# Kernel tuning notes

Measured on AMD Instinct MI355X. Metric: run time of the kernel, lower is better.

The kernel has to match this reference:

```python
import jax, jax.numpy as jnp
import numpy as np

NUM_HEADS = 24
HEAD_DIM = 64
SCALE = HEAD_DIM ** -0.5


def setup_inputs() -> dict:
    key = jax.random.key(0)
    ks = jax.random.split(key, 6)
    b, n_img, n_txt = 2, 4096, 128
    c_in, c_out, c_ctx = 1536, 1536, 4096
    x = jax.random.normal(ks[0], (b, n_img, c_in), dtype=jnp.float32)
    context = jax.random.normal(ks[1], (b, n_txt, c_ctx), dtype=jnp.float32)
    # realistic padding mask: first 96 of 128 tokens valid
    context_mask = jnp.broadcast_to(jnp.arange(n_txt) < 96, (b, n_txt))
    # Linear(in, out, bias=False) stored as [in, out] so y = x @ W
    Wq = jax.random.normal(ks[2], (c_in, c_out), dtype=jnp.float32) * (c_in ** -0.5)
    Wk = jax.random.normal(ks[3], (c_ctx, c_out), dtype=jnp.float32) * (c_ctx ** -0.5)
    Wv = jax.random.normal(ks[4], (c_ctx, c_out), dtype=jnp.float32) * (c_ctx ** -0.5)
    Wo = jax.random.normal(ks[5], (c_out, c_out), dtype=jnp.float32) * (c_out ** -0.5)
    return {"x": x, "context": context, "context_mask": context_mask,
            "Wq": Wq, "Wk": Wk, "Wv": Wv, "Wo": Wo}


def reference(x, context, context_mask, Wq, Wk, Wv, Wo):
    b, n, _ = x.shape
    h, d = NUM_HEADS, HEAD_DIM
    # project and split heads: b n (h d) -> b h n d
    q = (x @ Wq).reshape(b, n, h, d).transpose(0, 2, 1, 3)
    k = (context @ Wk).reshape(b, -1, h, d).transpose(0, 2, 1, 3)
    v = (context @ Wv).reshape(b, -1, h, d).transpose(0, 2, 1, 3)
    scores = jnp.einsum('bhid,bhjd->bhij', q, k) * SCALE
    max_neg = -jnp.finfo(scores.dtype).max
    scores = jnp.where(context_mask[:, None, None, :], scores, max_neg)
    attn = jax.nn.softmax(scores, axis=-1)
    out = jnp.einsum('bhij,bhjd->bhid', attn, v)
    out = out.transpose(0, 2, 1, 3).reshape(b, n, h * d)
    return out @ Wo
```

## Files before the change

### kernel.cpp

```cpp
#include <hip/hip_runtime.h>

typedef __attribute__((ext_vector_type(8))) short s8bf;
typedef __attribute__((ext_vector_type(8))) __bf16 v8bf;
typedef __attribute__((ext_vector_type(4))) float f32x4;

__device__ __forceinline__ short f2bf(float f) {
  union { float f; unsigned u; } v; v.f = f;
  unsigned r = v.u + 0x7FFFu + ((v.u >> 16) & 1u);
  return (short)(r >> 16);
}

__device__ __forceinline__ f32x4 mfma16(s8bf a, s8bf b, f32x4 c) {
  return __builtin_amdgcn_mfma_f32_16x16x32_bf16(
      __builtin_bit_cast(v8bf, a), __builtin_bit_cast(v8bf, b), c, 0, 0, 0);
}

__device__ __forceinline__ void gl_lds16(const void* g, void* l) {
  __builtin_amdgcn_global_load_lds(
      (const __attribute__((address_space(1))) unsigned*)g,
      (__attribute__((address_space(3))) unsigned*)l, 16, 0, 0);
}

__global__ void cvt_f32_bf16_k(const float* __restrict__ in, short* __restrict__ out, int n4) {
  int i = blockIdx.x * 256 + threadIdx.x;
  if (i < n4) {
    float4 v = ((const float4*)in)[i];
    short4 o;
    o.x = f2bf(v.x); o.y = f2bf(v.y); o.z = f2bf(v.z); o.w = f2bf(v.w);
    ((short4*)out)[i] = o;
  }
}

__global__ void transp_bf16_k(const float* __restrict__ W, short* __restrict__ Wt, int K, int N) {
  __shared__ float t[32][33];
  int k0 = blockIdx.x * 32, n0 = blockIdx.y * 32;
  int tx = threadIdx.x & 31, ty = threadIdx.x >> 5;
  #pragma unroll
  for (int i = 0; i < 4; ++i)
    t[ty + i * 8][tx] = W[(size_t)(k0 + ty + i * 8) * N + n0 + tx];
  __syncthreads();
  #pragma unroll
  for (int i = 0; i < 4; ++i)
    Wt[(size_t)(n0 + ty + i * 8) * K + k0 + tx] = f2bf(t[tx][ty + i * 8]);
}

__global__ void mask_bias_k(const void* __restrict__ mask, float* __restrict__ bias, int n) {
  __shared__ int fmt;
  const unsigned char* p8 = (const unsigned char*)mask;
  if (threadIdx.x == 0) {
    const float* pf = (const float*)mask;
    int allf = 1, anyone = 0;
    for (int i = 0; i < 64; ++i) {
      float f = pf[i];
      if (f != 0.0f && f != 1.0f) allf = 0;
      if (f == 1.0f) anyone = 1;
    }
    int any13 = 0;
    for (int i = 0; i < 256; ++i) if ((i & 3) && p8[i]) any13 = 1;
    fmt = (allf && anyone) ? 2 : (any13 ? 0 : 1);
  }
  __syncthreads();
  int j = threadIdx.x;
  if (j < n) {
    int m;
    if (fmt == 2)      m = (((const float*)mask)[j] != 0.0f);
    else if (fmt == 0) m = (p8[j] != 0);
    else               m = (((const int*)mask)[j] != 0);
    bias[j] = m ? 0.0f : -1e30f;
  }
}

template<int MODE>
__global__ __launch_bounds__(512, 2) void gemm8ph_k(
    const short* __restrict__ A, const short* __restrict__ Bt, void* __restrict__ C,
    int M, int N, int K)
{
  extern __shared__ char ldsb[];
  const int tid = threadIdx.x, wid = tid >> 6, lane = tid & 63;
  const int nbx = N / 192;
  const int nwg = gridDim.x, bid = blockIdx.x;
  const int swz = (bid & 7) * (nwg >> 3) + (bid >> 3);
  const int m0 = (swz / nbx) * 256, n0 = (swz % nbx) * 192;
  const int wm = wid >> 2, wn = wid & 3;
  const int NT = K / 64;

  const int sx  = (lane & 7) << 4;
  const int c0b = ((lane >> 4) * 16) ^ sx;
  const int c1b = ((lane >> 4) * 16 + 64) ^ sx;
  const int aoff0 = (wm * 128 + (lane & 15)) * 128 + c0b;
  const int aoff1 = (wm * 128 + (lane & 15)) * 128 + c1b;
  const int boff0 = 32768 + (wn * 48 + (lane & 15)) * 128 + c0b;
  const int boff1 = 32768 + (wn * 48 + (lane & 15)) * 128 + c1b;

  const int strow = tid >> 3;
  const int stcol = (16 * ((tid & 7) ^ ((tid >> 3) & 7))) >> 1;
  const short* sp[7];
  #pragma unroll
  for (int r = 0; r < 7; ++r) {
    if (r < 4) sp[r] = A  + (size_t)(m0 + r * 64 + strow) * K + stcol;
    else       sp[r] = Bt + (size_t)(n0 + (r - 4) * 64 + strow) * K + stcol;
  }

  f32x4 acc[8][3] = {};
  s8bf bfr[3][2];

  #pragma unroll
  for (int r = 0; r < 7; ++r) gl_lds16(sp[r], ldsb + r * 8192 + tid * 16);
  #pragma unroll
  for (int r = 0; r < 7; ++r) gl_lds16(sp[r] + 64, ldsb + 57344 + r * 8192 + tid * 16);
  asm volatile("s_waitcnt vmcnt(7)" ::: "memory");
  __builtin_amdgcn_s_barrier();

  for (int t = 0; t < NT; ++t) {
    const int bo = (t & 1) * 57344;
    const int so2 = ((t + 2) < NT ? (t + 2) : (NT - 1)) * 64;
    s8bf a0[4], a1[4], a2[4], a3[4];
    #pragma unroll
    for (int i = 0; i < 4; ++i) a0[i] = *(const s8bf*)(ldsb + bo + aoff0 + i * 2048);
    #pragma unroll
    for (int nf = 0; nf < 3; ++nf) bfr[nf][0] = *(const s8bf*)(ldsb + bo + boff0 + nf * 2048);
    #pragma unroll
    for (int i = 0; i < 4; ++i) a1[i] = *(const s8bf*)(ldsb + bo + aoff1 + i * 2048);
    #pragma unroll
    for (int nf = 0; nf < 3; ++nf) bfr[nf][1] = *(const s8bf*)(ldsb + bo + boff1 + nf * 2048);
    __builtin_amdgcn_s_barrier();
    asm volatile("s_waitcnt lgkmcnt(7)" ::: "memory");
    __builtin_amdgcn_s_setprio(1);
    #pragma unroll
    for (int i = 0; i < 4; ++i)
      #pragma unroll
      for (int nf = 0; nf < 3; ++nf)
        acc[i][nf] = mfma16(a0[i], bfr[nf][0], acc[i][nf]);
    __builtin_amdgcn_s_setprio(0);
    __builtin_amdgcn_s_barrier();
    #pragma unroll
    for (int i = 0; i < 4; ++i) a2[i] = *(const s8bf*)(ldsb + bo + aoff0 + (4 + i) * 2048);
    #pragma unroll
    for (int i = 0; i < 4; ++i) a3[i] = *(const s8bf*)(ldsb + bo + aoff1 + (4 + i) * 2048);
    __builtin_amdgcn_s_barrier();
    asm volatile("s_waitcnt lgkmcnt(8)" ::: "memory");
    __builtin_amdgcn_s_setprio(1);
    #pragma unroll
    for (int i = 0; i < 4; ++i)
      #pragma unroll
      for (int nf = 0; nf < 3; ++nf)
        acc[i][nf] = mfma16(a1[i], bfr[nf][1], acc[i][nf]);
    __builtin_amdgcn_s_setprio(0);
    asm volatile("s_waitcnt lgkmcnt(0)" ::: "memory");
    __builtin_amdgcn_s_barrier();
    #pragma unroll
    for (int r = 0; r < 4; ++r) gl_lds16(sp[r] + so2, ldsb + bo + r * 8192 + tid * 16);
    __builtin_amdgcn_s_barrier();
    __builtin_amdgcn_s_setprio(1);
    #pragma unroll
    for (int i = 0; i < 4; ++i)
      #pragma unroll
      for (int nf = 0; nf < 3; ++nf)
        acc[4 + i][nf] = mfma16(a2[i], bfr[nf][0], acc[4 + i][nf]);
    __builtin_amdgcn_s_setprio(0);
    __builtin_amdgcn_s_barrier();
    #pragma unroll
    for (int r = 4; r < 7; ++r) gl_lds16(sp[r] + so2, ldsb + bo + r * 8192 + tid * 16);
    __builtin_amdgcn_s_barrier();
    __builtin_amdgcn_s_setprio(1);
    #pragma unroll
    for (int i = 0; i < 4; ++i)
      #pragma unroll
      for (int nf = 0; nf < 3; ++nf)
        acc[4 + i][nf] = mfma16(a3[i], bfr[nf][1], acc[4 + i][nf]);
    __builtin_amdgcn_s_setprio(0);
    asm volatile("s_waitcnt vmcnt(7)" ::: "memory");
    __builtin_amdgcn_s_barrier();
  }
  asm volatile("s_waitcnt vmcnt(0)" ::: "memory");

  const int r0 = m0 + wm * 128 + ((lane >> 4) << 2);
  const int c0 = n0 + wn * 48 + (lane & 15);
  #pragma unroll
  for (int mf = 0; mf < 8; ++mf)
    #pragma unroll
    for (int nf = 0; nf < 3; ++nf)
      #pragma unroll
      for (int v = 0; v < 4; ++v) {
        int row = r0 + mf * 16 + v, col = c0 + nf * 16;
        float val = acc[mf][nf][v];
        if (MODE == 0) ((short*)C)[(size_t)row * N + col] = f2bf(val);
        else           ((float*)C)[(size_t)row * N + col] = val;
      }
}

template<int MODE>
__global__ __launch_bounds__(256, 2) void gemm_bt_k(
    const short* __restrict__ A, const short* __restrict__ Bt, void* __restrict__ C,
    int M, int N, int K, int kchunk)
{
  __shared__ short aT[128 * 32];
  __shared__ short bT[128 * 32];
  const int m0 = blockIdx.x * 128, n0 = blockIdx.y * 128;
  const int wid = threadIdx.x >> 6, lane = threadIdx.x & 63;
  const int wr = wid >> 1, wc = wid & 1;
  const int k_lo = blockIdx.z * kchunk, k_hi = k_lo + kchunk;
  f32x4 acc[4][4] = {};
  const int srow = wid * 32 + (lane >> 2);
  const int skoff = (lane & 3) * 8;
  const short* aG = A + (size_t)(m0 + srow) * K + skoff;
  const short* bG = Bt + (size_t)(n0 + srow) * K + skoff;
  char* aL = (char*)aT + wid * 2048;
  char* bL = (char*)bT + wid * 2048;
  const short* ap = aT + (wr * 64 + (lane & 15)) * 32 + (lane >> 4) * 8;
  const short* bp = bT + (wc * 64 + (lane & 15)) * 32 + (lane >> 4) * 8;
  for (int k0 = k_lo; k0 < k_hi; k0 += 32) {
    gl_lds16(aG + k0, aL);
    gl_lds16(aG + (size_t)16 * K + k0, aL + 1024);
    gl_lds16(bG + k0, bL);
    gl_lds16(bG + (size_t)16 * K + k0, bL + 1024);
    __syncthreads();
    s8bf af[4], bf[4];
    #pragma unroll
    for (int i = 0; i < 4; ++i) {
      af[i] = *(const s8bf*)(ap + i * 512);
      bf[i] = *(const s8bf*)(bp + i * 512);
    }
    #pragma unroll
    for (int mi = 0; mi < 4; ++mi)
      #pragma unroll
      for (int ni = 0; ni < 4; ++ni)
        acc[mi][ni] = mfma16(af[mi], bf[ni], acc[mi][ni]);
    __syncthreads();
  }
  const int r0 = m0 + wr * 64 + ((lane >> 4) << 2);
  const int c0 = n0 + wc * 64 + (lane & 15);
  float* Cf = (float*)C + (size_t)blockIdx.z * 786432;
  #pragma unroll
  for (int mi = 0; mi < 4; ++mi)
    #pragma unroll
    for (int ni = 0; ni < 4; ++ni)
      #pragma unroll
      for (int v = 0; v < 4; ++v) {
        int row = r0 + mi * 16 + v, col = c0 + ni * 16;
        Cf[(size_t)row * N + col] = acc[mi][ni][v];
      }
}

__global__ void kv_reduce_k(const float* __restrict__ part, short* __restrict__ kbf,
                            short* __restrict__ vtbf) {
  int t = blockIdx.x * 256 + threadIdx.x;
  int row = t / 768, c4 = (t % 768) * 4;
  float4 s = {0.f, 0.f, 0.f, 0.f};
  const float* p = part + (size_t)row * 3072 + c4;
  #pragma unroll
  for (int z = 0; z < 4; ++z) {
    float4 v = *(const float4*)(p + (size_t)z * 786432);
    s.x += v.x; s.y += v.y; s.z += v.z; s.w += v.w;
  }
  if (c4 < 1536) {
    short4 o = { f2bf(s.x), f2bf(s.y), f2bf(s.z), f2bf(s.w) };
    *(short4*)(kbf + (size_t)row * 1536 + c4) = o;
  } else {
    int b = row >> 7, j = row & 127, c = c4 - 1536;
    vtbf[((size_t)(b * 1536 + c + 0)) * 128 + j] = f2bf(s.x);
    vtbf[((size_t)(b * 1536 + c + 1)) * 128 + j] = f2bf(s.y);
    vtbf[((size_t)(b * 1536 + c + 2)) * 128 + j] = f2bf(s.z);
    vtbf[((size_t)(b * 1536 + c + 3)) * 128 + j] = f2bf(s.w);
  }
}

__global__ __launch_bounds__(256, 3) void attn_k(
    const short* __restrict__ q, const short* __restrict__ kk,
    const short* __restrict__ vt, const float* __restrict__ bias,
    short* __restrict__ ao)
{
  __shared__ char sm_[49152];
  const int it = blockIdx.x, h = blockIdx.y, b = blockIdx.z;
  const int wid = threadIdx.x >> 6, lane = threadIdx.x & 63;
  const int i0 = it * 128;
  char* kT = sm_;
  char* vT = sm_ + 16384;
  char* pB = (wid < 2) ? (sm_ + wid * 8192) : (sm_ + 16384 + wid * 8192);

  #pragma unroll
  for (int c = 0; c < 4; ++c) {
    int seg = c * 256 + wid * 64 + lane;
    int j = seg >> 3, ds = seg & 7;
    int dsrc = ds ^ (j & 7);
    gl_lds16(kk + ((size_t)(b * 128 + j) * 1536 + h * 64 + dsrc * 8),
             kT + c * 4096 + wid * 1024);
  }
  #pragma unroll
  for (int c = 0; c < 4; ++c) {
    int seg = c * 256 + wid * 64 + lane;
    int d = seg >> 4, js = seg & 15;
    int jsrc = js ^ (d & 7);
    gl_lds16(vt + ((size_t)(b * 1536 + h * 64 + d) * 128 + jsrc * 8),
             vT + c * 4096 + wid * 1024);
  }

  float bcol[8];
  #pragma unroll
  for (int nj = 0; nj < 8; ++nj) bcol[nj] = bias[b * 128 + nj * 16 + (lane & 15)];

  s8bf qf[2][2];
  #pragma unroll
  for (int mi = 0; mi < 2; ++mi)
    #pragma unroll
    for (int ks = 0; ks < 2; ++ks) {
      size_t row = (size_t)(b * 4096 + i0 + wid * 32 + mi * 16 + (lane & 15));
      qf[mi][ks] = *(const s8bf*)(q + row * 1536 + h * 64 + ks * 32 + (lane >> 4) * 8);
    }
  __syncthreads();

  f32x4 s[2][8] = {};
  #pragma unroll
  for (int ks = 0; ks < 2; ++ks) {
    int kd = ks * 32 + (lane >> 4) * 8;
    #pragma unroll
    for (int nj = 0; nj < 8; ++nj) {
      int j = nj * 16 + (lane & 15);
      s8bf kb = *(const s8bf*)(kT + j * 128 + ((2 * kd) ^ ((j & 7) << 4)));
      s[0][nj] = mfma16(qf[0][ks], kb, s[0][nj]);
      s[1][nj] = mfma16(qf[1][ks], kb, s[1][nj]);
    }
  }
  __syncthreads();

  float sm[2][4];
  #pragma unroll
  for (int mi = 0; mi < 2; ++mi)
    #pragma unroll
    for (int v = 0; v < 4; ++v) {
      float mx = -1e30f;
      #pragma unroll
      for (int nj = 0; nj < 8; ++nj) {
        float sv = s[mi][nj][v] * 0.125f + bcol[nj];
        s[mi][nj][v] = sv;
        mx = fmaxf(mx, sv);
      }
      mx = fmaxf(mx, __shfl_xor(mx, 1));
      mx = fmaxf(mx, __shfl_xor(mx, 2));
      mx = fmaxf(mx, __shfl_xor(mx, 4));
      mx = fmaxf(mx, __shfl_xor(mx, 8));
      float ss = 0.f;
      #pragma unroll
      for (int nj = 0; nj < 8; ++nj) {
        float p = __expf(s[mi][nj][v] - mx);
        s[mi][nj][v] = p;
        ss += p;
      }
      ss += __shfl_xor(ss, 1);
      ss += __shfl_xor(ss, 2);
      ss += __shfl_xor(ss, 4);
      ss += __shfl_xor(ss, 8);
      sm[mi][v] = ss;
    }

  #pragma unroll
  for (int mi = 0; mi < 2; ++mi)
    #pragma unroll
    for (int v = 0; v < 4; ++v) {
      int r = mi * 16 + ((lane >> 4) << 2) + v;
      char* base = pB + r * 256;
      #pragma unroll
      for (int nj = 0; nj < 8; ++nj) {
        int j = nj * 16 + (lane & 15);
        *(short*)(base + ((2 * j) ^ ((r & 7) << 4))) = f2bf(s[mi][nj][v]);
      }
    }
  __syncthreads();

  f32x4 o_[2][4] = {};
  #pragma unroll
  for (int ks = 0; ks < 4; ++ks) {
    int j = ks * 32 + (lane >> 4) * 8;
    s8bf pa[2];
    #pragma unroll
    for (int mi = 0; mi < 2; ++mi) {
      int r = mi * 16 + (lane & 15);
      pa[mi] = *(const s8bf*)(pB + r * 256 + ((2 * j) ^ ((r & 7) << 4)));
    }
    #pragma unroll
    for (int dj = 0; dj < 4; ++dj) {
      int d = dj * 16 + (lane & 15);
      s8bf vb = *(const s8bf*)(vT + d * 256 + ((2 * j) ^ ((d & 7) << 4)));
      o_[0][dj] = mfma16(pa[0], vb, o_[0][dj]);
      o_[1][dj] = mfma16(pa[1], vb, o_[1][dj]);
    }
  }

  #pragma unroll
  for (int mi = 0; mi < 2; ++mi)
    #pragma unroll
    for (int v = 0; v < 4; ++v) {
      int r = mi * 16 + ((lane >> 4) << 2) + v;
      float is = 1.0f / sm[mi][v];
      size_t row = (size_t)(b * 4096 + i0 + wid * 32 + r);
      #pragma unroll
      for (int dj = 0; dj < 4; ++dj) {
        int d = dj * 16 + (lane & 15);
        ao[row * 1536 + h * 64 + d] = f2bf(o_[mi][dj][v] * is);
      }
    }
}

extern "C" void kernel_launch(void* const* d_in, const int* in_sizes, int n_in,
                              void* d_out, int out_size, void* d_ws, size_t ws_size,
                              hipStream_t stream) {
  const float* x   = (const float*)d_in[0];
  const float* ctx = (const float*)d_in[1];
  const void*  msk = d_in[2];
  const float* Wq  = (const float*)d_in[3];
  const float* Wk  = (const float*)d_in[4];
  const float* Wv  = (const float*)d_in[5];
  const float* Wo  = (const float*)d_in[6];
  float* out = (float*)d_out;

  const int B = 2, NI = 4096, NT = 128, C = 1536, CC = 4096, H = 24;
  const int Mq = B * NI;
  const int Mk = B * NT;

  size_t off = 0;
  auto carve = [&](size_t bytes) -> void* {
    void* p = (char*)d_ws + off;
    off += (bytes + 255) & ~(size_t)255;
    return p;
  };
  short* xbf   = (short*)carve((size_t)Mq * C * 2);
  short* ctxbf = (short*)carve((size_t)Mk * CC * 2);
  short* WqT   = (short*)carve((size_t)C * C * 2);
  short* WkT   = (short*)carve((size_t)CC * C * 2);
  short* WvT   = (short*)carve((size_t)CC * C * 2);
  short* WoT   = (short*)carve((size_t)C * C * 2);
  short* qbf   = (short*)carve((size_t)Mq * C * 2);
  short* kbf   = (short*)carve((size_t)Mk * C * 2);
  short* vtbf  = (short*)carve((size_t)Mk * C * 2);
  float* bias  = (float*)carve(256 * 4);
  short* aout  = xbf;
  float* part  = out;

  hipFuncSetAttribute((const void*)gemm8ph_k<0>, hipFuncAttributeMaxDynamicSharedMemorySize, 114688);
  hipFuncSetAttribute((const void*)gemm8ph_k<1>, hipFuncAttributeMaxDynamicSharedMemorySize, 114688);

  cvt_f32_bf16_k<<<(Mq * C / 4 + 255) / 256, 256, 0, stream>>>(x, xbf, Mq * C / 4);
  cvt_f32_bf16_k<<<(Mk * CC / 4 + 255) / 256, 256, 0, stream>>>(ctx, ctxbf, Mk * CC / 4);
  transp_bf16_k<<<dim3(C / 32, C / 32), 256, 0, stream>>>(Wq, WqT, C, C);
  transp_bf16_k<<<dim3(CC / 32, C / 32), 256, 0, stream>>>(Wk, WkT, CC, C);
  transp_bf16_k<<<dim3(CC / 32, C / 32), 256, 0, stream>>>(Wv, WvT, CC, C);
  transp_bf16_k<<<dim3(C / 32, C / 32), 256, 0, stream>>>(Wo, WoT, C, C);
  mask_bias_k<<<1, 256, 0, stream>>>(msk, bias, 256);

  gemm8ph_k<0><<<(Mq / 256) * (C / 192), 512, 114688, stream>>>(xbf, WqT, qbf, Mq, C, C);
  gemm_bt_k<5><<<dim3(Mk / 128, 3072 / 128, 4), 256, 0, stream>>>(ctxbf, WkT, part, Mk, 3072, CC, 1024);
  kv_reduce_k<<<768, 256, 0, stream>>>(part, kbf, vtbf);

  attn_k<<<dim3(NI / 128, H, B), 256, 0, stream>>>(qbf, kbf, vtbf, bias, aout);

  gemm8ph_k<1><<<(Mq / 256) * (C / 192), 512, 114688, stream>>>(aout, WoT, out, Mq, C, C);
}
```

Baseline: 187.2 us.

## Rewrite projection GEMM with 256x256 tiles and four-phase split-K-half pipeline

Replaces the 256x192-tile eight-phase GEMM used for the Q and output projections with a 256x256-tile variant. This kernel splits each 64-wide K step into two 32-wide halves, each with its own XOR-swizzled LDS layout, and interleaves global-to-LDS prefetches of the next tiles between the MFMA phases. The larger N tile raises arithmetic intensity per LDS byte and reduces the workgroup count from 256 to 192. In exchange it uses 128 KB of LDS (possibly limiting occupancy to one block per CU), keeps more accumulators in registers, and leaves fewer workgroups than the 256 CUs, so some CUs sit idle.

Measured after the change: 198.9 us. 6.2% more time.

```diff
diff --git a/kernel.cpp b/kernel.cpp
--- a/kernel.cpp
+++ b/kernel.cpp
@@ -71,115 +71,129 @@
 }
 
 template<int MODE>
-__global__ __launch_bounds__(512, 2) void gemm8ph_k(
+__global__ __launch_bounds__(512, 2) void gemm4ph_k(
     const short* __restrict__ A, const short* __restrict__ Bt, void* __restrict__ C,
     int M, int N, int K)
 {
   extern __shared__ char ldsb[];
   const int tid = threadIdx.x, wid = tid >> 6, lane = tid & 63;
-  const int nbx = N / 192;
+  const int nbx = N / 256;
   const int nwg = gridDim.x, bid = blockIdx.x;
   const int swz = (bid & 7) * (nwg >> 3) + (bid >> 3);
-  const int m0 = (swz / nbx) * 256, n0 = (swz % nbx) * 192;
+  const int m0 = (swz / nbx) * 256, n0 = (swz % nbx) * 256;
   const int wm = wid >> 2, wn = wid & 3;
   const int NT = K / 64;
 
-  const int sx  = (lane & 7) << 4;
-  const int c0b = ((lane >> 4) * 16) ^ sx;
-  const int c1b = ((lane >> 4) * 16 + 64) ^ sx;
-  const int aoff0 = (wm * 128 + (lane & 15)) * 128 + c0b;
-  const int aoff1 = (wm * 128 + (lane & 15)) * 128 + c1b;
-  const int boff0 = 32768 + (wn * 48 + (lane & 15)) * 128 + c0b;
-  const int boff1 = 32768 + (wn * 48 + (lane & 15)) * 128 + c1b;
-
-  const int strow = tid >> 3;
-  const int stcol = (16 * ((tid & 7) ^ ((tid >> 3) & 7))) >> 1;
-  const short* sp[7];
-  #pragma unroll
-  for (int r = 0; r < 7; ++r) {
-    if (r < 4) sp[r] = A  + (size_t)(m0 + r * 64 + strow) * K + stcol;
-    else       sp[r] = Bt + (size_t)(n0 + (r - 4) * 64 + strow) * K + stcol;
-  }
-
-  f32x4 acc[8][3] = {};
-  s8bf bfr[3][2];
-
-  #pragma unroll
-  for (int r = 0; r < 7; ++r) gl_lds16(sp[r], ldsb + r * 8192 + tid * 16);
-  #pragma unroll
-  for (int r = 0; r < 7; ++r) gl_lds16(sp[r] + 64, ldsb + 57344 + r * 8192 + tid * 16);
-  asm volatile("s_waitcnt vmcnt(7)" ::: "memory");
+  const int cswz = 16 * ((lane >> 4) ^ (lane & 3) ^ ((lane >> 2) & 3));
+  int aoff[8], boff[4];
+  #pragma unroll
+  for (int mf = 0; mf < 8; ++mf)
+    aoff[mf] = (wm * 128 + mf * 16 + (lane & 15)) * 64 + cswz;
+  #pragma unroll
+  for (int nf = 0; nf < 4; ++nf)
+    boff[nf] = 32768 + (wn * 64 + nf * 16 + (lane & 15)) * 64 + cswz;
+
+  const int logslot = (lane & 3) ^ ((lane >> 2) & 3) ^ ((lane >> 4) & 3);
+  const int srow = wid * 32 + (lane >> 2);
+  const short* srcAg0 = A  + (size_t)(m0 + srow) * K + logslot * 8;
+  const short* srcAg1 = A  + (size_t)(m0 + srow + 16) * K + logslot * 8;
+  const short* srcBg0 = Bt + (size_t)(n0 + srow) * K + logslot * 8;
+  const short* srcBg1 = Bt + (size_t)(n0 + srow + 16) * K + logslot * 8;
+  const int dph = wid * 2048 + lane * 16;
+
+  f32x4 acc[8][4] = {};
+
+  gl_lds16(srcAg0,      ldsb + 0     + dph);
+  gl_lds16(srcAg1,      ldsb + 1024  + dph);
+  gl_lds16(srcAg0 + 32, ldsb + 16384 + dph);
+  gl_lds16(srcAg1 + 32, ldsb + 17408 + dph);
+  gl_lds16(srcBg0,      ldsb + 32768 + dph);
+  gl_lds16(srcBg1,      ldsb + 33792 + dph);
+  gl_lds16(srcBg0 + 32, ldsb + 49152 + dph);
+  gl_lds16(srcBg1 + 32, ldsb + 50176 + dph);
+  gl_lds16(srcAg0 + 64, ldsb + 65536 + 0     + dph);
+  gl_lds16(srcAg1 + 64, ldsb + 65536 + 1024  + dph);
+  gl_lds16(srcBg0 + 64, ldsb + 65536 + 32768 + dph);
+  gl_lds16(srcBg1 + 64, ldsb + 65536 + 33792 + dph);
+  asm volatile("s_waitcnt vmcnt(4)" ::: "memory");
   __builtin_amdgcn_s_barrier();
 
   for (int t = 0; t < NT; ++t) {
-    const int bo = (t & 1) * 57344;
-    const int so2 = ((t + 2) < NT ? (t + 2) : (NT - 1)) * 64;
-    s8bf a0[4], a1[4], a2[4], a3[4];
-    #pragma unroll
-    for (int i = 0; i < 4; ++i) a0[i] = *(const s8bf*)(ldsb + bo + aoff0 + i * 2048);
-    #pragma unroll
-    for (int nf = 0; nf < 3; ++nf) bfr[nf][0] = *(const s8bf*)(ldsb + bo + boff0 + nf * 2048);
-    #pragma unroll
-    for (int i = 0; i < 4; ++i) a1[i] = *(const s8bf*)(ldsb + bo + aoff1 + i * 2048);
-    #pragma unroll
-    for (int nf = 0; nf < 3; ++nf) bfr[nf][1] = *(const s8bf*)(ldsb + bo + boff1 + nf * 2048);
-    __builtin_amdgcn_s_barrier();
-    asm volatile("s_waitcnt lgkmcnt(7)" ::: "memory");
+    const int bo = (t & 1) * 65536, bo2 = bo ^ 65536;
+    const int kt1 = ((t + 1) < NT ? (t + 1) : (NT - 1)) * 64;
+    const int kt2 = ((t + 2) < NT ? (t + 2) : (NT - 1)) * 64;
+    s8bf av[4], bk[4];
+    #pragma unroll
+    for (int i = 0; i < 4; ++i) av[i] = *(const s8bf*)(ldsb + bo + aoff[i]);
+    #pragma unroll
+    for (int nf = 0; nf < 4; ++nf) bk[nf] = *(const s8bf*)(ldsb + bo + boff[nf]);
+    gl_lds16(srcAg0 + kt1 + 32, ldsb + bo2 + 16384 + dph);
+    gl_lds16(srcAg1 + kt1 + 32, ldsb + bo2 + 17408 + dph);
+    __builtin_amdgcn_s_barrier();
+    asm volatile("s_waitcnt lgkmcnt(0)" ::: "memory");
     __builtin_amdgcn_s_setprio(1);
     #pragma unroll
     for (int i = 0; i < 4; ++i)
       #pragma unroll
-      for (int nf = 0; nf < 3; ++nf)
-        acc[i][nf] = mfma16(a0[i], bfr[nf][0], acc[i][nf]);
+      for (int nf = 0; nf < 4; ++nf)
+        acc[i][nf] = mfma16(av[i], bk[nf], acc[i][nf]);
     __builtin_amdgcn_s_setprio(0);
     __builtin_amdgcn_s_barrier();
     #pragma unroll
-    for (int i = 0; i < 4; ++i) a2[i] = *(const s8bf*)(ldsb + bo + aoff0 + (4 + i) * 2048);
-    #pragma unroll
-    for (int i = 0; i < 4; ++i) a3[i] = *(const s8bf*)(ldsb + bo + aoff1 + (4 + i) * 2048);
-    __builtin_amdgcn_s_barrier();
-    asm volatile("s_waitcnt lgkmcnt(8)" ::: "memory");
+    for (int i = 0; i < 4; ++i) av[i] = *(const s8bf*)(ldsb + bo + aoff[4 + i]);
+    gl_lds16(srcBg0 + kt1 + 32, ldsb + bo2 + 49152 + dph);
+    gl_lds16(srcBg1 + kt1 + 32, ldsb + bo2 + 50176 + dph);
+    __builtin_amdgcn_s_barrier();
+    asm volatile("s_waitcnt lgkmcnt(0)" ::: "memory");
     __builtin_amdgcn_s_setprio(1);
     #pragma unroll
     for (int i = 0; i < 4; ++i)
       #pragma unroll
-      for (int nf = 0; nf < 3; ++nf)
-        acc[i][nf] = mfma16(a1[i], bfr[nf][1], acc[i][nf]);
+      for (int nf = 0; nf < 4; ++nf)
+        acc[4 + i][nf] = mfma16(av[i], bk[nf], acc[4 + i][nf]);
     __builtin_amdgcn_s_setprio(0);
+    asm volatile("s_waitcnt vmcnt(8)" ::: "memory");
+    __builtin_amdgcn_s_barrier();
+    #pragma unroll
+    for (int i = 0; i < 4; ++i) av[i] = *(const s8bf*)(ldsb + bo + 16384 + aoff[i]);
+    #pragma unroll
+    for (int nf = 0; nf < 4; ++nf) bk[nf] = *(const s8bf*)(ldsb + bo + 16384 + boff[nf]);
+    gl_lds16(srcAg0 + kt2, ldsb + bo + 0 + dph);
+    gl_lds16(srcAg1 + kt2, ldsb + bo + 1024 + dph);
+    __builtin_amdgcn_s_barrier();
     asm volatile("s_waitcnt lgkmcnt(0)" ::: "memory");
-    __builtin_amdgcn_s_barrier();
-    #pragma unroll
-    for (int r = 0; r < 4; ++r) gl_lds16(sp[r] + so2, ldsb + bo + r * 8192 + tid * 16);
-    __builtin_amdgcn_s_barrier();
     __builtin_amdgcn_s_setprio(1);
     #pragma unroll
     for (int i = 0; i < 4; ++i)
       #pragma unroll
-      for (int nf = 0; nf < 3; ++nf)
-        acc[4 + i][nf] = mfma16(a2[i], bfr[nf][0], acc[4 + i][nf]);
+      for (int nf = 0; nf < 4; ++nf)
+        acc[i][nf] = mfma16(av[i], bk[nf], acc[i][nf]);
     __builtin_amdgcn_s_setprio(0);
     __builtin_amdgcn_s_barrier();
     #pragma unroll
-    for (int r = 4; r < 7; ++r) gl_lds16(sp[r] + so2, ldsb + bo + r * 8192 + tid * 16);
-    __builtin_amdgcn_s_barrier();
+    for (int i = 0; i < 4; ++i) av[i] = *(const s8bf*)(ldsb + bo + 16384 + aoff[4 + i]);
+    gl_lds16(srcBg0 + kt2, ldsb + bo + 32768 + dph);
+    gl_lds16(srcBg1 + kt2, ldsb + bo + 33792 + dph);
+    __builtin_amdgcn_s_barrier();
+    asm volatile("s_waitcnt lgkmcnt(0)" ::: "memory");
     __builtin_amdgcn_s_setprio(1);
     #pragma unroll
     for (int i = 0; i < 4; ++i)
       #pragma unroll
-      for (int nf = 0; nf < 3; ++nf)
-        acc[4 + i][nf] = mfma16(a3[i], bfr[nf][1], acc[4 + i][nf]);
+      for (int nf = 0; nf < 4; ++nf)
+        acc[4 + i][nf] = mfma16(av[i], bk[nf], acc[4 + i][nf]);
     __builtin_amdgcn_s_setprio(0);
-    asm volatile("s_waitcnt vmcnt(7)" ::: "memory");
+    asm volatile("s_waitcnt vmcnt(8)" ::: "memory");
     __builtin_amdgcn_s_barrier();
   }
   asm volatile("s_waitcnt vmcnt(0)" ::: "memory");
 
   const int r0 = m0 + wm * 128 + ((lane >> 4) << 2);
-  const int c0 = n0 + wn * 48 + (lane & 15);
+  const int c0 = n0 + wn * 64 + (lane & 15);
   #pragma unroll
   for (int mf = 0; mf < 8; ++mf)
     #pragma unroll
-    for (int nf = 0; nf < 3; ++nf)
+    for (int nf = 0; nf < 4; ++nf)
       #pragma unroll
       for (int v = 0; v < 4; ++v) {
         int row = r0 + mf * 16 + v, col = c0 + nf * 16;
@@ -436,8 +450,8 @@
   short* aout  = xbf;
   float* part  = out;
 
-  hipFuncSetAttribute((const void*)gemm8ph_k<0>, hipFuncAttributeMaxDynamicSharedMemorySize, 114688);
-  hipFuncSetAttribute((const void*)gemm8ph_k<1>, hipFuncAttributeMaxDynamicSharedMemorySize, 114688);
+  hipFuncSetAttribute((const void*)gemm4ph_k<0>, hipFuncAttributeMaxDynamicSharedMemorySize, 131072);
+  hipFuncSetAttribute((const void*)gemm4ph_k<1>, hipFuncAttributeMaxDynamicSharedMemorySize, 131072);
 
   cvt_f32_bf16_k<<<(Mq * C / 4 + 255) / 256, 256, 0, stream>>>(x, xbf, Mq * C / 4);
   cvt_f32_bf16_k<<<(Mk * CC / 4 + 255) / 256, 256, 0, stream>>>(ctx, ctxbf, Mk * CC / 4);
@@ -447,11 +461,11 @@
   transp_bf16_k<<<dim3(C / 32, C / 32), 256, 0, stream>>>(Wo, WoT, C, C);
   mask_bias_k<<<1, 256, 0, stream>>>(msk, bias, 256);
 
-  gemm8ph_k<0><<<(Mq / 256) * (C / 192), 512, 114688, stream>>>(xbf, WqT, qbf, Mq, C, C);
+  gemm4ph_k<0><<<(Mq / 256) * (C / 256), 512, 131072, stream>>>(xbf, WqT, qbf, Mq, C, C);
   gemm_bt_k<5><<<dim3(Mk / 128, 3072 / 128, 4), 256, 0, stream>>>(ctxbf, WkT, part, Mk, 3072, CC, 1024);
   kv_reduce_k<<<768, 256, 0, stream>>>(part, kbf, vtbf);
 
   attn_k<<<dim3(NI / 128, H, B), 256, 0, stream>>>(qbf, kbf, vtbf, bias, aout);
 
-  gemm8ph_k<1><<<(Mq / 256) * (C / 192), 512, 114688, stream>>>(aout, WoT, out, Mq, C, C);
-}
+  gemm4ph_k<1><<<(Mq / 256) * (C / 256), 512, 131072, stream>>>(aout, WoT, out, Mq, C, C);
+}
```

## Rewrite projection GEMM with 32x32x16 MFMA and 256x256 tiles

Applied to the files above, without the earlier changes.

Replaces the 16x16x32 MFMA GEMM used for the Q and output projections with a kernel built on 32x32x16 bf16 MFMA. The block tile grows from 256x192 to 256x256, with a new swizzled LDS layout (two rows packed per 128-byte line) and 128 KB of double-buffered LDS. The main loop has fewer barriers: one stage per k-step instead of split A/B staging phases. The goal is more reuse per LDS load and less synchronisation overhead. In exchange, the launch drops to 192 workgroups, fewer than the CU count, and the larger LDS footprint limits residency to one block per CU.

New measurement: 206.7 us. +10.4%, slower.

```diff
diff --git a/kernel.cpp b/kernel.cpp
--- a/kernel.cpp
+++ b/kernel.cpp
@@ -3,6 +3,7 @@
 typedef __attribute__((ext_vector_type(8))) short s8bf;
 typedef __attribute__((ext_vector_type(8))) __bf16 v8bf;
 typedef __attribute__((ext_vector_type(4))) float f32x4;
+typedef __attribute__((ext_vector_type(16))) float f32x16;
 
 __device__ __forceinline__ short f2bf(float f) {
   union { float f; unsigned u; } v; v.f = f;
@@ -12,6 +13,11 @@
 
 __device__ __forceinline__ f32x4 mfma16(s8bf a, s8bf b, f32x4 c) {
   return __builtin_amdgcn_mfma_f32_16x16x32_bf16(
+      __builtin_bit_cast(v8bf, a), __builtin_bit_cast(v8bf, b), c, 0, 0, 0);
+}
+
+__device__ __forceinline__ f32x16 mfma32(s8bf a, s8bf b, f32x16 c) {
+  return __builtin_amdgcn_mfma_f32_32x32x16_bf16(
       __builtin_bit_cast(v8bf, a), __builtin_bit_cast(v8bf, b), c, 0, 0, 0);
 }
 
@@ -71,119 +77,132 @@
 }
 
 template<int MODE>
-__global__ __launch_bounds__(512, 2) void gemm8ph_k(
+__global__ __launch_bounds__(512, 2) void gemm32_k(
     const short* __restrict__ A, const short* __restrict__ Bt, void* __restrict__ C,
     int M, int N, int K)
 {
   extern __shared__ char ldsb[];
   const int tid = threadIdx.x, wid = tid >> 6, lane = tid & 63;
-  const int nbx = N / 192;
+  const int nbx = N / 256;
   const int nwg = gridDim.x, bid = blockIdx.x;
   const int swz = (bid & 7) * (nwg >> 3) + (bid >> 3);
-  const int m0 = (swz / nbx) * 256, n0 = (swz % nbx) * 192;
+  const int m0 = (swz / nbx) * 256, n0 = (swz % nbx) * 256;
   const int wm = wid >> 2, wn = wid & 3;
   const int NT = K / 64;
 
-  const int sx  = (lane & 7) << 4;
-  const int c0b = ((lane >> 4) * 16) ^ sx;
-  const int c1b = ((lane >> 4) * 16 + 64) ^ sx;
-  const int aoff0 = (wm * 128 + (lane & 15)) * 128 + c0b;
-  const int aoff1 = (wm * 128 + (lane & 15)) * 128 + c1b;
-  const int boff0 = 32768 + (wn * 48 + (lane & 15)) * 128 + c0b;
-  const int boff1 = 32768 + (wn * 48 + (lane & 15)) * 128 + c1b;
-
-  const int strow = tid >> 3;
-  const int stcol = (16 * ((tid & 7) ^ ((tid >> 3) & 7))) >> 1;
-  const short* sp[7];
-  #pragma unroll
-  for (int r = 0; r < 7; ++r) {
-    if (r < 4) sp[r] = A  + (size_t)(m0 + r * 64 + strow) * K + stcol;
-    else       sp[r] = Bt + (size_t)(n0 + (r - 4) * 64 + strow) * K + stcol;
-  }
-
-  f32x4 acc[8][3] = {};
-  s8bf bfr[3][2];
-
-  #pragma unroll
-  for (int r = 0; r < 7; ++r) gl_lds16(sp[r], ldsb + r * 8192 + tid * 16);
-  #pragma unroll
-  for (int r = 0; r < 7; ++r) gl_lds16(sp[r] + 64, ldsb + 57344 + r * 8192 + tid * 16);
-  asm volatile("s_waitcnt vmcnt(7)" ::: "memory");
+  const int lr = lane & 31;
+  const int hk = lane >> 5;
+  int aoff[4][2], boff[2][2];
+  #pragma unroll
+  for (int mf = 0; mf < 4; ++mf)
+    #pragma unroll
+    for (int p = 0; p < 2; ++p) {
+      int line = wm * 64 + mf * 16 + (lr >> 1);
+      int slot = (4 * (lr & 1) + p * 2 + hk) ^ (line & 7);
+      aoff[mf][p] = line * 128 + slot * 16;
+    }
+  #pragma unroll
+  for (int nf = 0; nf < 2; ++nf)
+    #pragma unroll
+    for (int p = 0; p < 2; ++p) {
+      int line = wn * 32 + nf * 16 + (lr >> 1);
+      int slot = (4 * (lr & 1) + p * 2 + hk) ^ (line & 7);
+      boff[nf][p] = 32768 + line * 128 + slot * 16;
+    }
+
+  const int ls = (tid & 7) ^ ((tid >> 3) & 7);
+  const int srow2 = 2 * (tid >> 3) + (ls >> 2);
+  const int scol = (ls & 3) * 8;
+  const short* sA_lo = A  + (size_t)(m0 + srow2) * K + scol;
+  const short* sA_hi = A  + (size_t)(m0 + 128 + srow2) * K + scol;
+  const short* sB_lo = Bt + (size_t)(n0 + srow2) * K + scol;
+  const short* sB_hi = Bt + (size_t)(n0 + 128 + srow2) * K + scol;
+  const int d16 = tid * 16;
+
+  auto stage = [&](int koff, int bo_) {
+    gl_lds16(sA_lo + koff,      ldsb + bo_ + 0     + d16);
+    gl_lds16(sA_hi + koff,      ldsb + bo_ + 8192  + d16);
+    gl_lds16(sA_lo + koff + 32, ldsb + bo_ + 16384 + d16);
+    gl_lds16(sA_hi + koff + 32, ldsb + bo_ + 24576 + d16);
+    gl_lds16(sB_lo + koff,      ldsb + bo_ + 32768 + d16);
+    gl_lds16(sB_hi + koff,      ldsb + bo_ + 40960 + d16);
+    gl_lds16(sB_lo + koff + 32, ldsb + bo_ + 49152 + d16);
+    gl_lds16(sB_hi + koff + 32, ldsb + bo_ + 57344 + d16);
+  };
+
+  f32x16 acc[4][2] = {};
+  s8bf a0[4], a1[4], b0[2], b1[2];
+
+  stage(0, 0);
+  stage(((1 < NT) ? 1 : 0) * 64, 65536);
+  asm volatile("s_waitcnt vmcnt(8)" ::: "memory");
   __builtin_amdgcn_s_barrier();
 
   for (int t = 0; t < NT; ++t) {
-    const int bo = (t & 1) * 57344;
-    const int so2 = ((t + 2) < NT ? (t + 2) : (NT - 1)) * 64;
-    s8bf a0[4], a1[4], a2[4], a3[4];
-    #pragma unroll
-    for (int i = 0; i < 4; ++i) a0[i] = *(const s8bf*)(ldsb + bo + aoff0 + i * 2048);
-    #pragma unroll
-    for (int nf = 0; nf < 3; ++nf) bfr[nf][0] = *(const s8bf*)(ldsb + bo + boff0 + nf * 2048);
-    #pragma unroll
-    for (int i = 0; i < 4; ++i) a1[i] = *(const s8bf*)(ldsb + bo + aoff1 + i * 2048);
-    #pragma unroll
-    for (int nf = 0; nf < 3; ++nf) bfr[nf][1] = *(const s8bf*)(ldsb + bo + boff1 + nf * 2048);
-    __builtin_amdgcn_s_barrier();
-    asm volatile("s_waitcnt lgkmcnt(7)" ::: "memory");
+    const int bo = (t & 1) * 65536;
+    const int kt2 = ((t + 2) < NT ? (t + 2) : (NT - 1)) * 64;
+    #pragma unroll
+    for (int mf = 0; mf < 4; ++mf) a0[mf] = *(const s8bf*)(ldsb + bo + aoff[mf][0]);
+    #pragma unroll
+    for (int nf = 0; nf < 2; ++nf) b0[nf] = *(const s8bf*)(ldsb + bo + boff[nf][0]);
+    #pragma unroll
+    for (int mf = 0; mf < 4; ++mf) a1[mf] = *(const s8bf*)(ldsb + bo + aoff[mf][1]);
+    #pragma unroll
+    for (int nf = 0; nf < 2; ++nf) b1[nf] = *(const s8bf*)(ldsb + bo + boff[nf][1]);
     __builtin_amdgcn_s_setprio(1);
     #pragma unroll
-    for (int i = 0; i < 4; ++i)
-      #pragma unroll
-      for (int nf = 0; nf < 3; ++nf)
-        acc[i][nf] = mfma16(a0[i], bfr[nf][0], acc[i][nf]);
+    for (int mf = 0; mf < 4; ++mf)
+      #pragma unroll
+      for (int nf = 0; nf < 2; ++nf)
+        acc[mf][nf] = mfma32(a0[mf], b0[nf], acc[mf][nf]);
+    __builtin_amdgcn_s_setprio(0);
+    #pragma unroll
+    for (int mf = 0; mf < 4; ++mf) a0[mf] = *(const s8bf*)(ldsb + bo + 16384 + aoff[mf][0]);
+    #pragma unroll
+    for (int nf = 0; nf < 2; ++nf) b0[nf] = *(const s8bf*)(ldsb + bo + 16384 + boff[nf][0]);
+    __builtin_amdgcn_s_setprio(1);
+    #pragma unroll
+    for (int mf = 0; mf < 4; ++mf)
+      #pragma unroll
+      for (int nf = 0; nf < 2; ++nf)
+        acc[mf][nf] = mfma32(a1[mf], b1[nf], acc[mf][nf]);
+    __builtin_amdgcn_s_setprio(0);
+    #pragma unroll
+    for (int mf = 0; mf < 4; ++mf) a1[mf] = *(const s8bf*)(ldsb + bo + 16384 + aoff[mf][1]);
+    #pragma unroll
+    for (int nf = 0; nf < 2; ++nf) b1[nf] = *(const s8bf*)(ldsb + bo + 16384 + boff[nf][1]);
+    __builtin_amdgcn_s_setprio(1);
+    #pragma unroll
+    for (int mf = 0; mf < 4; ++mf)
+      #pragma unroll
+      for (int nf = 0; nf < 2; ++nf)
+        acc[mf][nf] = mfma32(a0[mf], b0[nf], acc[mf][nf]);
+    __builtin_amdgcn_s_setprio(0);
+    __builtin_amdgcn_s_setprio(1);
+    #pragma unroll
+    for (int mf = 0; mf < 4; ++mf)
+      #pragma unroll
+      for (int nf = 0; nf < 2; ++nf)
+        acc[mf][nf] = mfma32(a1[mf], b1[nf], acc[mf][nf]);
     __builtin_amdgcn_s_setprio(0);
     __builtin_amdgcn_s_barrier();
-    #pragma unroll
-    for (int i = 0; i < 4; ++i) a2[i] = *(const s8bf*)(ldsb + bo + aoff0 + (4 + i) * 2048);
-    #pragma unroll
-    for (int i = 0; i < 4; ++i) a3[i] = *(const s8bf*)(ldsb + bo + aoff1 + (4 + i) * 2048);
+    stage(kt2, bo);
+    asm volatile("s_waitcnt vmcnt(8)" ::: "memory");
     __builtin_amdgcn_s_barrier();
-    asm volatile("s_waitcnt lgkmcnt(8)" ::: "memory");
-    __builtin_amdgcn_s_setprio(1);
-    #pragma unroll
-    for (int i = 0; i < 4; ++i)
-      #pragma unroll
-      for (int nf = 0; nf < 3; ++nf)
-        acc[i][nf] = mfma16(a1[i], bfr[nf][1], acc[i][nf]);
-    __builtin_amdgcn_s_setprio(0);
-    asm volatile("s_waitcnt lgkmcnt(0)" ::: "memory");
-    __builtin_amdgcn_s_barrier();
-    #pragma unroll
-    for (int r = 0; r < 4; ++r) gl_lds16(sp[r] + so2, ldsb + bo + r * 8192 + tid * 16);
-    __builtin_amdgcn_s_barrier();
-    __builtin_amdgcn_s_setprio(1);
-    #pragma unroll
-    for (int i = 0; i < 4; ++i)
-      #pragma unroll
-      for (int nf = 0; nf < 3; ++nf)
-        acc[4 + i][nf] = mfma16(a2[i], bfr[nf][0], acc[4 + i][nf]);
-    __builtin_amdgcn_s_setprio(0);
-    __builtin_amdgcn_s_barrier();
-    #pragma unroll
-    for (int r = 4; r < 7; ++r) gl_lds16(sp[r] + so2, ldsb + bo + r * 8192 + tid * 16);
-    __builtin_amdgcn_s_barrier();
-    __builtin_amdgcn_s_setprio(1);
-    #pragma unroll
-    for (int i = 0; i < 4; ++i)
-      #pragma unroll
-      for (int nf = 0; nf < 3; ++nf)
-        acc[4 + i][nf] = mfma16(a3[i], bfr[nf][1], acc[4 + i][nf]);
-    __builtin_amdgcn_s_setprio(0);
-    asm volatile("s_waitcnt vmcnt(7)" ::: "memory");
-    __builtin_amdgcn_s_barrier();
   }
   asm volatile("s_waitcnt vmcnt(0)" ::: "memory");
 
-  const int r0 = m0 + wm * 128 + ((lane >> 4) << 2);
-  const int c0 = n0 + wn * 48 + (lane & 15);
-  #pragma unroll
-  for (int mf = 0; mf < 8; ++mf)
-    #pragma unroll
-    for (int nf = 0; nf < 3; ++nf)
-      #pragma unroll
-      for (int v = 0; v < 4; ++v) {
-        int row = r0 + mf * 16 + v, col = c0 + nf * 16;
-        float val = acc[mf][nf][v];
+  const int rb = m0 + wm * 128 + 4 * hk;
+  const int cb = n0 + wn * 64 + lr;
+  #pragma unroll
+  for (int mf = 0; mf < 4; ++mf)
+    #pragma unroll
+    for (int nf = 0; nf < 2; ++nf)
+      #pragma unroll
+      for (int r = 0; r < 16; ++r) {
+        int row = rb + mf * 32 + (r & 3) + 8 * (r >> 2);
+        int col = cb + nf * 32;
+        float val = acc[mf][nf][r];
         if (MODE == 0) ((short*)C)[(size_t)row * N + col] = f2bf(val);
         else           ((float*)C)[(size_t)row * N + col] = val;
       }
@@ -436,8 +455,8 @@
   short* aout  = xbf;
   float* part  = out;
 
-  hipFuncSetAttribute((const void*)gemm8ph_k<0>, hipFuncAttributeMaxDynamicSharedMemorySize, 114688);
-  hipFuncSetAttribute((const void*)gemm8ph_k<1>, hipFuncAttributeMaxDynamicSharedMemorySize, 114688);
+  hipFuncSetAttribute((const void*)gemm32_k<0>, hipFuncAttributeMaxDynamicSharedMemorySize, 131072);
+  hipFuncSetAttribute((const void*)gemm32_k<1>, hipFuncAttributeMaxDynamicSharedMemorySize, 131072);
 
   cvt_f32_bf16_k<<<(Mq * C / 4 + 255) / 256, 256, 0, stream>>>(x, xbf, Mq * C / 4);
   cvt_f32_bf16_k<<<(Mk * CC / 4 + 255) / 256, 256, 0, stream>>>(ctx, ctxbf, Mk * CC / 4);
@@ -447,11 +466,11 @@
   transp_bf16_k<<<dim3(C / 32, C / 32), 256, 0, stream>>>(Wo, WoT, C, C);
   mask_bias_k<<<1, 256, 0, stream>>>(msk, bias, 256);
 
-  gemm8ph_k<0><<<(Mq / 256) * (C / 192), 512, 114688, stream>>>(xbf, WqT, qbf, Mq, C, C);
+  gemm32_k<0><<<(Mq / 256) * (C / 256), 512, 131072, stream>>>(xbf, WqT, qbf, Mq, C, C);
   gemm_bt_k<5><<<dim3(Mk / 128, 3072 / 128, 4), 256, 0, stream>>>(ctxbf, WkT, part, Mk, 3072, CC, 1024);
   kv_reduce_k<<<768, 256, 0, stream>>>(part, kbf, vtbf);
 
   attn_k<<<dim3(NI / 128, H, B), 256, 0, stream>>>(qbf, kbf, vtbf, bias, aout);
 
-  gemm8ph_k<1><<<(Mq / 256) * (C / 192), 512, 114688, stream>>>(aout, WoT, out, Mq, C, C);
-}
+  gemm32_k<1><<<(Mq / 256) * (C / 256), 512, 131072, stream>>>(aout, WoT, out, Mq, C, C);
+}
```
